# Kernel optimization log

Hardware: AMD Instinct MI355X
Metric: run time of the kernel (lower is better)

## Reference

```python
import jax, jax.numpy as jnp
import numpy as np

N_FEATS = 64   # channels (n_feats)
P = 32         # het-conv period: (j - i) % P == 0 -> 3x3 kernel, else 1x1
BATCH, H, W = 16, 256, 256


def setup_inputs() -> dict:
    key = jax.random.key(0)
    k1, k2, k3, k4 = jax.random.split(key, 4)
    x = jax.random.normal(k1, (BATCH, N_FEATS, H, W), dtype=jnp.float32)
    # One 1x1-or-3x3 single-channel conv per (out_chan i, in_chan j) pair.
    # We store full dense tensors; a (i,j) mask inside reference() selects
    # which entries actually exist in the original module.
    w3 = jax.random.normal(k2, (N_FEATS, N_FEATS, 3, 3), dtype=jnp.float32) * 0.1
    w1 = jax.random.normal(k3, (N_FEATS, N_FEATS, 1, 1), dtype=jnp.float32) * 0.1
    # Each of the n_feats^2 Conv2d(1,1) has a bias; summing over j per output
    # channel i collapses them into a single per-output-channel bias.
    b = jax.random.normal(k4, (N_FEATS,), dtype=jnp.float32) * 0.1
    return {"x": x, "w3": w3, "w1": w1, "b": b}


def reference(x, w3, w1, b):
    C = w3.shape[0]
    i = jnp.arange(C)[:, None]  # out channel
    j = jnp.arange(C)[None, :]  # in channel
    m3 = ((j - i) % P == 0).astype(w3.dtype)  # [C, C] 1 where 3x3 kernel used
    # Fuse the n_feats^2 tiny convs into one dense OIHW kernel: 3x3 taps where
    # mask is on, 1x1 weight embedded at the 3x3 center elsewhere (pad=1 makes
    # the embedded 1x1 exactly equal to a stride-1 pad-0 1x1 conv).
    Wk = w3 * m3[:, :, None, None]
    Wk = Wk.at[:, :, 1, 1].add(w1[:, :, 0, 0] * (1.0 - m3))
    y = jax.lax.conv_general_dilated(
        x, Wk, window_strides=(1, 1), padding=((1, 1), (1, 1)),
        dimension_numbers=("NCHW", "OIHW", "NCHW"))
    return y + b[None, :, None, None]
```

## Files before the change

### kernel.cpp

```cpp
#include <hip/hip_runtime.h>


#define HH 256
#define WW 256
#define CCH 64
#define HW (HH * WW)
#define NB 16
#define PH 258
#define PW 258
#define TH 4
#define TW 32
#define HROWS (TH + 2)
#define HCOLS (TW + 2)
#define NPIX (HROWS * HCOLS)
#define ROWB (HCOLS * CCH * 2)
#define NCHUNK (NPIX * 8)

#define CHS 36
#define RSTR (CCH * CHS)
#define SMEM_BYTES (TH * RSTR * 4)

#define XQ_BYTES ((size_t)NB * PH * PW * CCH * 2)
#define NSLOT 22
#define FRAG_BYTES (2 * NSLOT * 64 * 16)

typedef __attribute__((ext_vector_type(8))) short bf16x8;
typedef __attribute__((ext_vector_type(4))) float f32x4;
typedef __attribute__((ext_vector_type(4))) unsigned int u32x4;

typedef __attribute__((address_space(1))) const unsigned int gu32;
typedef __attribute__((address_space(3))) unsigned int lu32;

__device__ __forceinline__ unsigned short f2bf(float f) {
    unsigned int u = __float_as_uint(f);
    u += 0x7FFFu + ((u >> 16) & 1u);
    return (unsigned short)(u >> 16);
}

__global__ __launch_bounds__(128) void build_frags(
    const float* __restrict__ w3, const float* __restrict__ w1,
    const float* __restrict__ b, u32x4* __restrict__ frag)
{
    const int tid = threadIdx.x;
    if (tid >= 128) return;
    const int pair = tid >> 6;
    const int lane = tid & 63;
    const int l15  = lane & 15;
    const int lq   = lane >> 4;

    const int ia = pair * 16 + l15;
    const int ib = ia + 32;

    u32x4* out = frag + (size_t)pair * NSLOT * 64 + lane;

    #pragma unroll
    for (int mt = 0; mt < 2; ++mt) {
        const int i = mt ? ib : ia;
        #pragma unroll
        for (int kh = 0; kh < 2; ++kh) {
            const int c0 = kh * 32 + lq * 8;
            bf16x8 v;
            #pragma unroll
            for (int e = 0; e < 8; ++e) {
                const int j = c0 + e;
                const float wval = (((j ^ i) & 31) == 0)
                                   ? w3[((size_t)i * CCH + j) * 9 + 4]
                                   : w1[(size_t)i * CCH + j];
                v[e] = (short)f2bf(wval);
            }
            out[(mt * 2 + kh) * 64] = __builtin_bit_cast(u32x4, v);
        }
    }

    const bool avalid = ((lq & 1) == (l15 >> 3));
    const int  epos   = l15 & 7;
    const int  jcol   = pair * 16 + l15 + 32 * (lane >> 5);
    #pragma unroll
    for (int mt = 0; mt < 2; ++mt) {
        const int i = mt ? ib : ia;
        const float* wp = w3 + ((size_t)i * CCH + jcol) * 9;
        int ti = 0;
        #pragma unroll
        for (int t = 0; t < 9; ++t) {
            if (t == 4) continue;
            const float val = avalid ? wp[t] : 0.0f;
            const short bv = (short)f2bf(val);
            bf16x8 f;
            #pragma unroll
            for (int e2 = 0; e2 < 8; ++e2) f[e2] = (e2 == epos) ? bv : (short)0;
            out[(4 + mt * 8 + ti) * 64] = __builtin_bit_cast(u32x4, f);
            ++ti;
        }
    }

    #pragma unroll
    for (int mt = 0; mt < 2; ++mt) {
        const int chb = (mt ? 32 : 0) + pair * 16 + lq * 4;
        f32x4 bv = (f32x4){b[chb + 0], b[chb + 1], b[chb + 2], b[chb + 3]};
        out[(20 + mt) * 64] = __builtin_bit_cast(u32x4, bv);
    }
}

__global__ __launch_bounds__(256) void prepass(
    const float* __restrict__ x, unsigned short* __restrict__ xq)
{
    __shared__ __align__(16) unsigned short s[256 * CCH];
    const int t  = threadIdx.x;
    const int hp = blockIdx.x;
    const int n  = blockIdx.y;
    char* sb = (char*)s;
    unsigned short* rowp = xq + ((size_t)(n * PH + hp)) * PW * CCH;
    const int NCH16 = PW * CCH / 8;

    if (hp == 0 || hp == PH - 1) {
        const u32x4 z = (u32x4){0u, 0u, 0u, 0u};
        for (int i = t; i < NCH16; i += 256)
            *(u32x4*)((char*)rowp + (size_t)i * 16) = z;
        return;
    }

    const int h = hp - 1;
    const float* xp = x + (size_t)n * CCH * HW + (size_t)h * WW + t;
    #pragma unroll 4
    for (int c4 = 0; c4 < CCH; c4 += 4) {
        float v0 = __builtin_nontemporal_load(xp + (size_t)(c4 + 0) * HW);
        float v1 = __builtin_nontemporal_load(xp + (size_t)(c4 + 1) * HW);
        float v2 = __builtin_nontemporal_load(xp + (size_t)(c4 + 2) * HW);
        float v3 = __builtin_nontemporal_load(xp + (size_t)(c4 + 3) * HW);
        uint2 pk;
        pk.x = (unsigned)f2bf(v0) | ((unsigned)f2bf(v1) << 16);
        pk.y = (unsigned)f2bf(v2) | ((unsigned)f2bf(v3) << 16);
        *(uint2*)(sb + (t << 7) + ((c4 << 1) ^ ((t & 7) << 4))) = pk;
    }
    __syncthreads();

    for (int i = t; i < NCH16; i += 256) {
        const int wp = i >> 3;
        const int s8 = i & 7;
        u32x4 v;
        if (wp == 0 || wp == PW - 1) {
            v = (u32x4){0u, 0u, 0u, 0u};
        } else {
            const int r = wp - 1;
            const int cslot = s8 ^ (wp & 7);
            v = *(const u32x4*)(sb + (r << 7) + ((cslot ^ (r & 7)) << 4));
        }
        *(u32x4*)((char*)rowp + (size_t)i * 16) = v;
    }
}

__global__ __launch_bounds__(256, 3) void hetconv_main(
    const unsigned short* __restrict__ xq, const u32x4* __restrict__ frag,
    float* __restrict__ y)
{
    __shared__ __align__(16) char smem[SMEM_BYTES];

    const int tid  = threadIdx.x;
    const int lane = tid & 63;
    const int wv   = tid >> 6;
    const int l15  = lane & 15;
    const int lq   = lane >> 4;
    const int pair  = wv & 1;
    const int trow0 = (wv >> 1) * 2;

    const int n  = blockIdx.z;
    const int h0 = blockIdx.y * TH;
    const int w0 = blockIdx.x * TW;
    const size_t nbase = (size_t)n * CCH * HW;

    {
        const unsigned short* gsrc =
            xq + ((size_t)(n * PH + h0) * PW + w0) * CCH;
        #pragma unroll
        for (int it = 0; it < 7; ++it) {
            const int ck = it * 256 + tid;
            if (it < 6 || tid < (NCHUNK - 6 * 256)) {
                const int r = ck / (HCOLS * 8);
                const int o = ck - r * (HCOLS * 8);
                const unsigned short* gp = gsrc + (size_t)r * PW * CCH + o * 8;
                __builtin_amdgcn_global_load_lds(
                    (gu32*)(const void*)gp,
                    (lu32*)(void*)(smem + ck * 16), 16, 0, 0);
            }
        }
    }

    __syncthreads();

    const char* lbase = (const char*)smem;
    const u32x4* fb = frag + (size_t)pair * NSLOT * 64 + lane;
    const int c0t = pair * 16 + (lq & 1) * 8 + 32 * (lane >> 5);

    f32x4 acc[4][2];
    #pragma unroll
    for (int g = 0; g < 4; ++g)
        #pragma unroll
        for (int mt = 0; mt < 2; ++mt)
            acc[g][mt] = (f32x4){0.f, 0.f, 0.f, 0.f};

    #pragma unroll
    for (int kh = 0; kh < 2; ++kh) {
        const bf16x8 f0 = __builtin_bit_cast(bf16x8, fb[(0 * 2 + kh) * 64]);
        const bf16x8 f1 = __builtin_bit_cast(bf16x8, fb[(1 * 2 + kh) * 64]);
        const int c = kh * 32 + lq * 8;
        #pragma unroll
        for (int g = 0; g < 4; ++g) {
            const int row = trow0 + (g >> 1);
            const int p   = (g & 1) * 16 + l15 + 1;
            const bf16x8 bf = *(const bf16x8*)(lbase + (row + 1) * ROWB + (p << 7)
                                               + ((c << 1) ^ ((p & 7) << 4)));
            acc[g][0] = __builtin_amdgcn_mfma_f32_16x16x32_bf16(f0, bf, acc[g][0], 0, 0, 0);
            acc[g][1] = __builtin_amdgcn_mfma_f32_16x16x32_bf16(f1, bf, acc[g][1], 0, 0, 0);
        }
    }

    {
        int ti = 0;
        #pragma unroll
        for (int t = 0; t < 9; ++t) {
            if (t == 4) continue;
            const int dy = t / 3, dx = t % 3;
            const bf16x8 f0 = __builtin_bit_cast(bf16x8, fb[(4 + ti) * 64]);
            const bf16x8 f1 = __builtin_bit_cast(bf16x8, fb[(4 + 8 + ti) * 64]);
            #pragma unroll
            for (int g = 0; g < 4; ++g) {
                const int row = trow0 + (g >> 1);
                const int p   = (g & 1) * 16 + l15 + dx;
                const bf16x8 bf = *(const bf16x8*)(lbase + (row + dy) * ROWB + (p << 7)
                                                   + ((c0t << 1) ^ ((p & 7) << 4)));
                acc[g][0] = __builtin_amdgcn_mfma_f32_16x16x32_bf16(f0, bf, acc[g][0], 0, 0, 0);
                acc[g][1] = __builtin_amdgcn_mfma_f32_16x16x32_bf16(f1, bf, acc[g][1], 0, 0, 0);
            }
            ++ti;
        }
    }

    f32x4 bias_[2];
    #pragma unroll
    for (int mt = 0; mt < 2; ++mt)
        bias_[mt] = __builtin_bit_cast(f32x4, fb[(20 + mt) * 64]);

    __syncthreads();
    float* sy = (float*)smem;
    #pragma unroll
    for (int g = 0; g < 4; ++g) {
        const int row = trow0 + (g >> 1);
        const int px  = (g & 1) * 16 + l15;
        #pragma unroll
        for (int mt = 0; mt < 2; ++mt) {
            const int chb = (mt ? 32 : 0) + pair * 16 + lq * 4;
            #pragma unroll
            for (int r = 0; r < 4; ++r) {
                sy[row * RSTR + (chb + r) * CHS + px] = acc[g][mt][r] + bias_[mt][r];
            }
        }
    }
    __syncthreads();

    #pragma unroll
    for (int i2 = 0; i2 < 8; ++i2) {
        const int idx = i2 * 256 + tid;
        const int row = idx >> 9;
        const int rem = idx & 511;
        const int ch  = rem >> 3;
        const int q   = rem & 7;
        const f32x4 v = *(const f32x4*)(sy + row * RSTR + ch * CHS + q * 4);
        float* dst = y + nbase + (size_t)ch * HW + (size_t)(h0 + row) * WW + w0 + q * 4;
        __builtin_nontemporal_store(v, (f32x4*)dst);
    }
}

__global__ __launch_bounds__(256, 2) void hetconv_mfma(
    const float* __restrict__ x, const float* __restrict__ w3,
    const float* __restrict__ w1, const float* __restrict__ b,
    float* __restrict__ y)
{
    __shared__ __align__(16) unsigned short s_x[NPIX * CCH];

    const int tid  = threadIdx.x;
    const int lane = tid & 63;
    const int wv   = tid >> 6;
    const int l15  = lane & 15;
    const int lq   = lane >> 4;
    const int pair  = wv & 1;
    const int trow0 = (wv >> 1) * 2;

    const int n  = blockIdx.z;
    const int h0 = blockIdx.y * TH;
    const int w0 = blockIdx.x * TW;
    const size_t nbase = (size_t)n * CCH * HW;

    if (tid < NPIX) {
        const int r = tid / HCOLS;
        const int c = tid - r * HCOLS;
        const int gh = h0 + r - 1;
        const int gw = w0 + c - 1;
        const bool inb = ((unsigned)gh < HH) && ((unsigned)gw < WW);
        const float* xp = x + nbase + (size_t)(inb ? gh : 0) * WW + (inb ? gw : 0);
        char* lbase = (char*)s_x;
        #pragma unroll 4
        for (int c4 = 0; c4 < CCH; c4 += 4) {
            float v0 = inb ? xp[(size_t)(c4 + 0) * HW] : 0.0f;
            float v1 = inb ? xp[(size_t)(c4 + 1) * HW] : 0.0f;
            float v2 = inb ? xp[(size_t)(c4 + 2) * HW] : 0.0f;
            float v3 = inb ? xp[(size_t)(c4 + 3) * HW] : 0.0f;
            uint2 pk;
            pk.x = (unsigned)f2bf(v0) | ((unsigned)f2bf(v1) << 16);
            pk.y = (unsigned)f2bf(v2) | ((unsigned)f2bf(v3) << 16);
            *(uint2*)(lbase + (tid << 7) + ((c4 << 1) ^ ((tid & 7) << 4))) = pk;
        }
    }

    const int ia = pair * 16 + l15;
    const int ib = ia + 32;
    bf16x8 fc[2][2];
    #pragma unroll
    for (int mt = 0; mt < 2; ++mt) {
        const int i = mt ? ib : ia;
        #pragma unroll
        for (int kh = 0; kh < 2; ++kh) {
            const int c0 = kh * 32 + lq * 8;
            bf16x8 v;
            #pragma unroll
            for (int e = 0; e < 8; ++e) {
                const int j = c0 + e;
                const float wval = (((j ^ i) & 31) == 0)
                                   ? w3[((size_t)i * CCH + j) * 9 + 4]
                                   : w1[(size_t)i * CCH + j];
                v[e] = (short)f2bf(wval);
            }
            fc[mt][kh] = v;
        }
    }
    const bool avalid = ((lq & 1) == (l15 >> 3));
    const int  epos   = l15 & 7;
    const int  jcol   = pair * 16 + l15 + 32 * (lane >> 5);
    bf16x8 ft[2][8];
    #pragma unroll
    for (int mt = 0; mt < 2; ++mt) {
        const int i = mt ? ib : ia;
        const float* wp = w3 + ((size_t)i * CCH + jcol) * 9;
        int ti = 0;
        #pragma unroll
        for (int t = 0; t < 9; ++t) {
            if (t == 4) continue;
            const float val = avalid ? wp[t] : 0.0f;
            const short bv = (short)f2bf(val);
            bf16x8 f;
            #pragma unroll
            for (int e2 = 0; e2 < 8; ++e2) f[e2] = (e2 == epos) ? bv : (short)0;
            ft[mt][ti] = f;
            ++ti;
        }
    }
    float bias_[2][4];
    #pragma unroll
    for (int mt = 0; mt < 2; ++mt) {
        const int chb = (mt ? 32 : 0) + pair * 16 + lq * 4;
        #pragma unroll
        for (int r = 0; r < 4; ++r) bias_[mt][r] = b[chb + r];
    }
    __syncthreads();

    const char* lbase = (const char*)s_x;
    const int c0t = pair * 16 + (lq & 1) * 8 + 32 * (lane >> 5);
    f32x4 acc[4][2];
    #pragma unroll
    for (int g = 0; g < 4; ++g)
        #pragma unroll
        for (int mt = 0; mt < 2; ++mt)
            acc[g][mt] = (f32x4){0.f, 0.f, 0.f, 0.f};

    #pragma unroll
    for (int g = 0; g < 4; ++g) {
        const int row = trow0 + (g >> 1);
        const int gc  = (g & 1) * 16;
        {
            const int p = (row + 1) * HCOLS + gc + l15 + 1;
            #pragma unroll
            for (int kh = 0; kh < 2; ++kh) {
                const int c = kh * 32 + lq * 8;
                const bf16x8 bf = *(const bf16x8*)(lbase + (p << 7) + ((c << 1) ^ ((p & 7) << 4)));
                acc[g][0] = __builtin_amdgcn_mfma_f32_16x16x32_bf16(fc[0][kh], bf, acc[g][0], 0, 0, 0);
                acc[g][1] = __builtin_amdgcn_mfma_f32_16x16x32_bf16(fc[1][kh], bf, acc[g][1], 0, 0, 0);
            }
        }
        int ti = 0;
        #pragma unroll
        for (int t = 0; t < 9; ++t) {
            if (t == 4) continue;
            const int dy = t / 3, dx = t % 3;
            const int p = (row + dy) * HCOLS + gc + l15 + dx;
            const bf16x8 bf = *(const bf16x8*)(lbase + (p << 7) + ((c0t << 1) ^ ((p & 7) << 4)));
            acc[g][0] = __builtin_amdgcn_mfma_f32_16x16x32_bf16(ft[0][ti], bf, acc[g][0], 0, 0, 0);
            acc[g][1] = __builtin_amdgcn_mfma_f32_16x16x32_bf16(ft[1][ti], bf, acc[g][1], 0, 0, 0);
            ++ti;
        }
    }

    #pragma unroll
    for (int g = 0; g < 4; ++g) {
        const int row = trow0 + (g >> 1);
        const int gc  = (g & 1) * 16;
        const int gh  = h0 + row;
        const int gw  = w0 + gc + l15;
        #pragma unroll
        for (int mt = 0; mt < 2; ++mt) {
            const int chb = (mt ? 32 : 0) + pair * 16 + lq * 4;
            #pragma unroll
            for (int r = 0; r < 4; ++r) {
                y[nbase + (size_t)(chb + r) * HW + (size_t)gh * WW + gw] =
                    acc[g][mt][r] + bias_[mt][r];
            }
        }
    }
}

extern "C" void kernel_launch(void* const* d_in, const int* in_sizes, int n_in,
                              void* d_out, int out_size, void* d_ws, size_t ws_size,
                              hipStream_t stream) {
    (void)in_sizes; (void)n_in; (void)out_size;
    const float* x  = (const float*)d_in[0];
    const float* w3 = (const float*)d_in[1];
    const float* w1 = (const float*)d_in[2];
    const float* b  = (const float*)d_in[3];
    float* y = (float*)d_out;

    const size_t need = XQ_BYTES + FRAG_BYTES;
    if (ws_size >= need) {
        unsigned short* xq = (unsigned short*)d_ws;
        u32x4* frag = (u32x4*)((char*)d_ws + XQ_BYTES);
        hipLaunchKernelGGL(build_frags, dim3(1, 1, 1), dim3(128, 1, 1), 0, stream,
                           w3, w1, b, frag);
        hipLaunchKernelGGL(prepass, dim3(PH, NB, 1), dim3(256, 1, 1), 0, stream, x, xq);
        hipLaunchKernelGGL(hetconv_main, dim3(WW / TW, HH / TH, NB), dim3(256, 1, 1),
                           0, stream, xq, frag, y);
    } else {
        hipLaunchKernelGGL(hetconv_mfma, dim3(WW / TW, HH / TH, NB), dim3(256, 1, 1),
                           0, stream, x, w3, w1, b, y);
    }
}
```

Baseline: 146.1 us.

## Fuse bf16 transpose prepass into conv kernel, loading fp32 NCHW tiles directly

Removes the separate prepass that wrote a padded bf16 NHWC copy of the input to workspace. The conv kernel now reads fp32 NCHW halo tiles straight from x with float4 loads, converts them to bf16, and writes them into swizzled LDS using a 40-column halo aligned to 4 pixels. Border zeros are produced by predication. Launch bounds rise to 4 blocks per CU. This drops a full write and re-read of the bf16 intermediate, but each block now reloads wider halos from fp32 and does the conversion inline.

```diff
diff --git a/kernel.cpp b/kernel.cpp
--- a/kernel.cpp
+++ b/kernel.cpp
@@ -6,30 +6,23 @@
 #define CCH 64
 #define HW (HH * WW)
 #define NB 16
-#define PH 258
-#define PW 258
 #define TH 4
 #define TW 32
-#define HROWS (TH + 2)
-#define HCOLS (TW + 2)
-#define NPIX (HROWS * HCOLS)
-#define ROWB (HCOLS * CCH * 2)
-#define NCHUNK (NPIX * 8)
+#define SROWS 6
+#define SCOLS 40
+#define ROWB2 (SCOLS * CCH * 2)
+#define NGRP 960
 
 #define CHS 36
 #define RSTR (CCH * CHS)
 #define SMEM_BYTES (TH * RSTR * 4)
 
-#define XQ_BYTES ((size_t)NB * PH * PW * CCH * 2)
 #define NSLOT 22
 #define FRAG_BYTES (2 * NSLOT * 64 * 16)
 
 typedef __attribute__((ext_vector_type(8))) short bf16x8;
 typedef __attribute__((ext_vector_type(4))) float f32x4;
 typedef __attribute__((ext_vector_type(4))) unsigned int u32x4;
-
-typedef __attribute__((address_space(1))) const unsigned int gu32;
-typedef __attribute__((address_space(3))) unsigned int lu32;
 
 __device__ __forceinline__ unsigned short f2bf(float f) {
     unsigned int u = __float_as_uint(f);
@@ -42,7 +35,6 @@
     const float* __restrict__ b, u32x4* __restrict__ frag)
 {
     const int tid = threadIdx.x;
-    if (tid >= 128) return;
     const int pair = tid >> 6;
     const int lane = tid & 63;
     const int l15  = lane & 15;
@@ -101,56 +93,8 @@
     }
 }
 
-__global__ __launch_bounds__(256) void prepass(
-    const float* __restrict__ x, unsigned short* __restrict__ xq)
-{
-    __shared__ __align__(16) unsigned short s[256 * CCH];
-    const int t  = threadIdx.x;
-    const int hp = blockIdx.x;
-    const int n  = blockIdx.y;
-    char* sb = (char*)s;
-    unsigned short* rowp = xq + ((size_t)(n * PH + hp)) * PW * CCH;
-    const int NCH16 = PW * CCH / 8;
-
-    if (hp == 0 || hp == PH - 1) {
-        const u32x4 z = (u32x4){0u, 0u, 0u, 0u};
-        for (int i = t; i < NCH16; i += 256)
-            *(u32x4*)((char*)rowp + (size_t)i * 16) = z;
-        return;
-    }
-
-    const int h = hp - 1;
-    const float* xp = x + (size_t)n * CCH * HW + (size_t)h * WW + t;
-    #pragma unroll 4
-    for (int c4 = 0; c4 < CCH; c4 += 4) {
-        float v0 = __builtin_nontemporal_load(xp + (size_t)(c4 + 0) * HW);
-        float v1 = __builtin_nontemporal_load(xp + (size_t)(c4 + 1) * HW);
-        float v2 = __builtin_nontemporal_load(xp + (size_t)(c4 + 2) * HW);
-        float v3 = __builtin_nontemporal_load(xp + (size_t)(c4 + 3) * HW);
-        uint2 pk;
-        pk.x = (unsigned)f2bf(v0) | ((unsigned)f2bf(v1) << 16);
-        pk.y = (unsigned)f2bf(v2) | ((unsigned)f2bf(v3) << 16);
-        *(uint2*)(sb + (t << 7) + ((c4 << 1) ^ ((t & 7) << 4))) = pk;
-    }
-    __syncthreads();
-
-    for (int i = t; i < NCH16; i += 256) {
-        const int wp = i >> 3;
-        const int s8 = i & 7;
-        u32x4 v;
-        if (wp == 0 || wp == PW - 1) {
-            v = (u32x4){0u, 0u, 0u, 0u};
-        } else {
-            const int r = wp - 1;
-            const int cslot = s8 ^ (wp & 7);
-            v = *(const u32x4*)(sb + (r << 7) + ((cslot ^ (r & 7)) << 4));
-        }
-        *(u32x4*)((char*)rowp + (size_t)i * 16) = v;
-    }
-}
-
-__global__ __launch_bounds__(256, 3) void hetconv_main(
-    const unsigned short* __restrict__ xq, const u32x4* __restrict__ frag,
+__global__ __launch_bounds__(256, 4) void hetconv_fused(
+    const float* __restrict__ x, const u32x4* __restrict__ frag,
     float* __restrict__ y)
 {
     __shared__ __align__(16) char smem[SMEM_BYTES];
@@ -168,19 +112,37 @@
     const int w0 = blockIdx.x * TW;
     const size_t nbase = (size_t)n * CCH * HW;
 
-    {
-        const unsigned short* gsrc =
-            xq + ((size_t)(n * PH + h0) * PW + w0) * CCH;
-        #pragma unroll
-        for (int it = 0; it < 7; ++it) {
-            const int ck = it * 256 + tid;
-            if (it < 6 || tid < (NCHUNK - 6 * 256)) {
-                const int r = ck / (HCOLS * 8);
-                const int o = ck - r * (HCOLS * 8);
-                const unsigned short* gp = gsrc + (size_t)r * PW * CCH + o * 8;
-                __builtin_amdgcn_global_load_lds(
-                    (gu32*)(const void*)gp,
-                    (lu32*)(void*)(smem + ck * 16), 16, 0, 0);
+    #pragma unroll
+    for (int it = 0; it < 4; ++it) {
+        const int gi = it * 256 + tid;
+        if (gi < NGRP) {
+            const int c4  = gi & 15;
+            const int rs  = gi >> 4;
+            const int r   = rs / 10;
+            const int sub = rs - r * 10;
+            const int gh  = h0 + r - 1;
+            const int gw0 = w0 - 4 + sub * 4;
+            const bool valid = ((unsigned)gh < (unsigned)HH) &&
+                               ((unsigned)gw0 <= (unsigned)(WW - 4));
+            const int ghc = valid ? gh : 0;
+            const int gwc = valid ? gw0 : 0;
+            const float* xp = x + nbase + (size_t)(c4 * 4) * HW + (size_t)ghc * WW + gwc;
+            f32x4 q0 = *(const f32x4*)(xp + 0 * (size_t)HW);
+            f32x4 q1 = *(const f32x4*)(xp + 1 * (size_t)HW);
+            f32x4 q2 = *(const f32x4*)(xp + 2 * (size_t)HW);
+            f32x4 q3 = *(const f32x4*)(xp + 3 * (size_t)HW);
+            if (!valid) {
+                q0 = (f32x4){0.f, 0.f, 0.f, 0.f};
+                q1 = q0; q2 = q0; q3 = q0;
+            }
+            char* rbase = smem + r * ROWB2;
+            #pragma unroll
+            for (int k = 0; k < 4; ++k) {
+                const int p = sub * 4 + k;
+                uint2 pk;
+                pk.x = (unsigned)f2bf(q0[k]) | ((unsigned)f2bf(q1[k]) << 16);
+                pk.y = (unsigned)f2bf(q2[k]) | ((unsigned)f2bf(q3[k]) << 16);
+                *(uint2*)(rbase + (p << 7) + ((c4 * 8) ^ ((p & 7) << 4))) = pk;
             }
         }
     }
@@ -206,8 +168,8 @@
         #pragma unroll
         for (int g = 0; g < 4; ++g) {
             const int row = trow0 + (g >> 1);
-            const int p   = (g & 1) * 16 + l15 + 1;
-            const bf16x8 bf = *(const bf16x8*)(lbase + (row + 1) * ROWB + (p << 7)
+            const int p   = (g & 1) * 16 + l15 + 4;
+            const bf16x8 bf = *(const bf16x8*)(lbase + (row + 1) * ROWB2 + (p << 7)
                                                + ((c << 1) ^ ((p & 7) << 4)));
             acc[g][0] = __builtin_amdgcn_mfma_f32_16x16x32_bf16(f0, bf, acc[g][0], 0, 0, 0);
             acc[g][1] = __builtin_amdgcn_mfma_f32_16x16x32_bf16(f1, bf, acc[g][1], 0, 0, 0);
@@ -225,8 +187,8 @@
             #pragma unroll
             for (int g = 0; g < 4; ++g) {
                 const int row = trow0 + (g >> 1);
-                const int p   = (g & 1) * 16 + l15 + dx;
-                const bf16x8 bf = *(const bf16x8*)(lbase + (row + dy) * ROWB + (p << 7)
+                const int p   = (g & 1) * 16 + l15 + dx + 3;
+                const bf16x8 bf = *(const bf16x8*)(lbase + (row + dy) * ROWB2 + (p << 7)
                                                    + ((c0t << 1) ^ ((p & 7) << 4)));
                 acc[g][0] = __builtin_amdgcn_mfma_f32_16x16x32_bf16(f0, bf, acc[g][0], 0, 0, 0);
                 acc[g][1] = __builtin_amdgcn_mfma_f32_16x16x32_bf16(f1, bf, acc[g][1], 0, 0, 0);
@@ -269,6 +231,10 @@
         __builtin_nontemporal_store(v, (f32x4*)dst);
     }
 }
+
+#define HROWS (TH + 2)
+#define HCOLS (TW + 2)
+#define NPIX (HROWS * HCOLS)
 
 __global__ __launch_bounds__(256, 2) void hetconv_mfma(
     const float* __restrict__ x, const float* __restrict__ w3,
@@ -426,15 +392,12 @@
     const float* b  = (const float*)d_in[3];
     float* y = (float*)d_out;
 
-    const size_t need = XQ_BYTES + FRAG_BYTES;
-    if (ws_size >= need) {
-        unsigned short* xq = (unsigned short*)d_ws;
-        u32x4* frag = (u32x4*)((char*)d_ws + XQ_BYTES);
+    if (ws_size >= (size_t)FRAG_BYTES) {
+        u32x4* frag = (u32x4*)d_ws;
         hipLaunchKernelGGL(build_frags, dim3(1, 1, 1), dim3(128, 1, 1), 0, stream,
                            w3, w1, b, frag);
-        hipLaunchKernelGGL(prepass, dim3(PH, NB, 1), dim3(256, 1, 1), 0, stream, x, xq);
-        hipLaunchKernelGGL(hetconv_main, dim3(WW / TW, HH / TH, NB), dim3(256, 1, 1),
-                           0, stream, xq, frag, y);
+        hipLaunchKernelGGL(hetconv_fused, dim3(WW / TW, HH / TH, NB), dim3(256, 1, 1),
+                           0, stream, x, frag, y);
     } else {
         hipLaunchKernelGGL(hetconv_mfma, dim3(WW / TW, HH / TH, NB), dim3(256, 1, 1),
                            0, stream, x, w3, w1, b, y);
```

After: 201.9 us. 38.2% more time.
